# Kernel tuning notes

Measured on AMD Instinct MI355X. Metric: run time of the kernel, lower is better.

The kernel has to match this reference:

```python
import jax, jax.numpy as jnp
import numpy as np

TTT_LR = 0.01
LN_EPS = 1e-5


def setup_inputs() -> dict:
    key = jax.random.key(0)
    ks = jax.random.split(key, 4)
    B, S, D, DS = 4, 2048, 1024, 64
    sc = 1.0 / np.sqrt(D).astype(np.float32)
    return {
        "x": jax.random.normal(ks[0], (B, S, D), dtype=jnp.float32),
        "Wk": jax.random.normal(ks[1], (DS, D), dtype=jnp.float32) * sc,
        "bk": jnp.zeros((DS,), jnp.float32),
        "Wv": jax.random.normal(ks[2], (D, D), dtype=jnp.float32) * sc,
        "bv": jnp.zeros((D,), jnp.float32),
        "Wq": jax.random.normal(ks[3], (DS, D), dtype=jnp.float32) * sc,
        "bq": jnp.zeros((DS,), jnp.float32),
        "gamma": jnp.ones((D,), jnp.float32),
        "beta": jnp.zeros((D,), jnp.float32),
    }


def reference(x, Wk, bk, Wv, bv, Wq, bq, gamma, beta):
    B, S, D = x.shape
    DS = Wk.shape[0]
    # LayerNorm over last dim
    mu = jnp.mean(x, axis=-1, keepdims=True)
    var = jnp.mean((x - mu) ** 2, axis=-1, keepdims=True)
    h = (x - mu) * jax.lax.rsqrt(var + LN_EPS) * gamma + beta
    # projections: keys/queries (B,S,DS), values (B,S,D)
    keys = jnp.einsum('bsd,ed->bse', h, Wk) + bk
    values = jnp.einsum('bsd,ed->bse', h, Wv) + bv
    queries = jnp.einsum('bsd,ed->bse', h, Wq) + bq

    def step(W, qkv):
        # W: (B, D, DS) fast-weight state
        q_t, k_t, v_t = qkv  # (B,DS), (B,DS), (B,D)
        y_t = jnp.einsum('bds,bs->bd', W, q_t)      # read with query
        pred = jnp.einsum('bds,bs->bd', W, k_t)     # predict with key
        err = pred - v_t                             # (B, D)
        W = W - TTT_LR * err[:, :, None] * k_t[:, None, :]  # rank-1 grad step
        return W, y_t

    W0 = jnp.zeros((B, D, DS), x.dtype)
    # scan over time: inputs as (S, B, ...)
    qs = jnp.swapaxes(queries, 0, 1)
    ks_ = jnp.swapaxes(keys, 0, 1)
    vs = jnp.swapaxes(values, 0, 1)
    _, ys = jax.lax.scan(step, W0, (qs, ks_, vs))   # ys: (S, B, D)
    y = jnp.swapaxes(ys, 0, 1)
    return x + y
```

## Files before the change

### kernel.cpp

```cpp
#include <hip/hip_runtime.h>
#include <hip/hip_bf16.h>

#define TTT_LR 0.01f
#define LN_EPS 1e-5f

#define BB 4
#define SS 2048
#define DD 1024
#define DSZ 64
#define CHUNK 64
#define NC (SS / CHUNK)
#define NCAT 1152
#define NCVT (NCAT * DD / 4 / 256)
#define MiB (1024ull * 1024ull)

typedef __hip_bfloat16 bf16;
typedef __bf16 bf16x8 __attribute__((ext_vector_type(8)));
typedef float f32x4 __attribute__((ext_vector_type(4)));

__device__ __forceinline__ void gload_lds16(const void* g, void* l) {
    __builtin_amdgcn_global_load_lds(
        (const __attribute__((address_space(1))) unsigned int*)g,
        (__attribute__((address_space(3))) unsigned int*)l, 16, 0, 0);
}

__global__ __launch_bounds__(256) void pre_kernel(
    const float* __restrict__ Wk, const float* __restrict__ Wq,
    const float* __restrict__ Wv, bf16* __restrict__ Wcat,
    const float* __restrict__ x, const float* __restrict__ gamma,
    const float* __restrict__ beta, bf16* __restrict__ hb)
{
    __shared__ float wsum[4], wsum2[4];
    const int tid = threadIdx.x;

    if (blockIdx.x < NCVT) {
        const int i = blockIdx.x * 256 + tid;
        const int idx = i * 4;
        const int row = idx >> 10, col = idx & 1023;
        const float* src = (row < 64)  ? (Wk + (size_t)row * DD)
                         : (row < 128) ? (Wq + (size_t)(row - 64) * DD)
                                       : (Wv + (size_t)(row - 128) * DD);
        float4 v = *reinterpret_cast<const float4*>(src + col);
        bf16 h4[4] = {__float2bfloat16(v.x), __float2bfloat16(v.y),
                      __float2bfloat16(v.z), __float2bfloat16(v.w)};
        *reinterpret_cast<ushort4*>(Wcat + idx) = *reinterpret_cast<ushort4*>(h4);
        return;
    }

    const int row = blockIdx.x - NCVT;
    const int lane = tid & 63, wave = tid >> 6;

    float4 v0 = *reinterpret_cast<const float4*>(x + (size_t)row * DD + tid * 4);
    float s = v0.x + v0.y + v0.z + v0.w;
    float s2 = fmaf(v0.x, v0.x, fmaf(v0.y, v0.y, fmaf(v0.z, v0.z, v0.w * v0.w)));
    #pragma unroll
    for (int off = 32; off > 0; off >>= 1) {
        s  += __shfl_down(s, off, 64);
        s2 += __shfl_down(s2, off, 64);
    }
    if (lane == 0) { wsum[wave] = s; wsum2[wave] = s2; }
    __syncthreads();
    s  = wsum[0] + wsum[1] + wsum[2] + wsum[3];
    s2 = wsum2[0] + wsum2[1] + wsum2[2] + wsum2[3];
    const float mu = s * (1.0f / DD);
    const float rs = rsqrtf(s2 * (1.0f / DD) - mu * mu + LN_EPS);

    float4 g  = *reinterpret_cast<const float4*>(gamma + tid * 4);
    float4 be = *reinterpret_cast<const float4*>(beta + tid * 4);
    bf16 h4[4];
    h4[0] = __float2bfloat16((v0.x - mu) * rs * g.x + be.x);
    h4[1] = __float2bfloat16((v0.y - mu) * rs * g.y + be.y);
    h4[2] = __float2bfloat16((v0.z - mu) * rs * g.z + be.z);
    h4[3] = __float2bfloat16((v0.w - mu) * rs * g.w + be.w);
    *reinterpret_cast<ushort4*>(hb + (size_t)row * DD + tid * 4) =
        *reinterpret_cast<ushort4*>(h4);
}

__global__ __launch_bounds__(256) void kqv_kernel(
    const bf16* __restrict__ h, const bf16* __restrict__ Wcat,
    const float* __restrict__ bk, const float* __restrict__ bq,
    const float* __restrict__ bv,
    float* __restrict__ kbuf, float* __restrict__ qbuf, bf16* __restrict__ vbuf16)
{
    __shared__ bf16 Ash[64 * 64];
    __shared__ bf16 Bsh[128 * 64];
    const int tid = threadIdx.x, lane = tid & 63, wave = tid >> 6;
    const int m = lane & 15, quad = lane >> 4;
    const int wr = wave >> 1, wc = wave & 1;

    const int id = blockIdx.x;
    const int tile = (id & 7) * 144 + (id >> 3);
    const int mtile = tile / 9;
    const int ntile = tile % 9;
    const int m0 = mtile * 64;
    const int n0 = ntile * 128;

    const int srow = wave * 8 + (lane >> 3);
    const int scb = lane & 7;

    f32x4 acc[2][4] = {};

    for (int k0 = 0; k0 < DD; k0 += 64) {
        __syncthreads();
        #pragma unroll
        for (int i = 0; i < 2; ++i) {
            const int row = i * 32 + srow;
            const int g16 = scb ^ (row & 7);
            gload_lds16(h    + (size_t)(m0 + row) * DD + k0 + g16 * 8,
                        (char*)Ash + (size_t)(i * 32 + wave * 8) * 128);
        }
        #pragma unroll
        for (int i = 0; i < 4; ++i) {
            const int row = i * 32 + srow;
            const int g16 = scb ^ (row & 7);
            gload_lds16(Wcat + (size_t)(n0 + row) * DD + k0 + g16 * 8,
                        (char*)Bsh + (size_t)(i * 32 + wave * 8) * 128);
        }
        __syncthreads();
        #pragma unroll
        for (int ks = 0; ks < 2; ++ks) {
            bf16x8 af[2], bfr[4];
            #pragma unroll
            for (int mt = 0; mt < 2; ++mt) {
                const int row = wr * 32 + mt * 16 + m;
                const int kb = (ks * 4 + quad) ^ (row & 7);
                af[mt] = *reinterpret_cast<const bf16x8*>(&Ash[row * 64 + kb * 8]);
            }
            #pragma unroll
            for (int nt = 0; nt < 4; ++nt) {
                const int row = wc * 64 + nt * 16 + m;
                const int kb = (ks * 4 + quad) ^ (row & 7);
                bfr[nt] = *reinterpret_cast<const bf16x8*>(&Bsh[row * 64 + kb * 8]);
            }
            #pragma unroll
            for (int mt = 0; mt < 2; ++mt)
                #pragma unroll
                for (int nt = 0; nt < 4; ++nt)
                    acc[mt][nt] = __builtin_amdgcn_mfma_f32_16x16x32_bf16(
                        af[mt], bfr[nt], acc[mt][nt], 0, 0, 0);
        }
    }

    #pragma unroll
    for (int nt = 0; nt < 4; ++nt) {
        const int n = n0 + wc * 64 + nt * 16 + m;
        if (n < 64) {
            const float bias = bk[n];
            #pragma unroll
            for (int mt = 0; mt < 2; ++mt) {
                const int row = m0 + wr * 32 + mt * 16 + quad * 4;
                #pragma unroll
                for (int r = 0; r < 4; ++r)
                    kbuf[(size_t)(row + r) * DSZ + n] = acc[mt][nt][r] + bias;
            }
        } else if (n < 128) {
            const float bias = bq[n - 64];
            #pragma unroll
            for (int mt = 0; mt < 2; ++mt) {
                const int row = m0 + wr * 32 + mt * 16 + quad * 4;
                #pragma unroll
                for (int r = 0; r < 4; ++r)
                    qbuf[(size_t)(row + r) * DSZ + (n - 64)] = acc[mt][nt][r] + bias;
            }
        } else {
            const float bias = bv[n - 128];
            #pragma unroll
            for (int mt = 0; mt < 2; ++mt) {
                const int row = m0 + wr * 32 + mt * 16 + quad * 4;
                #pragma unroll
                for (int r = 0; r < 4; ++r)
                    vbuf16[(size_t)(row + r) * DD + (n - 128)] =
                        __float2bfloat16(acc[mt][nt][r] + bias);
            }
        }
    }
}

__global__ __launch_bounds__(256) void prep_kernel(
    const float* __restrict__ kbuf, const float* __restrict__ qbuf,
    bf16* __restrict__ Tb16, bf16* __restrict__ Wb16,
    bf16* __restrict__ AMb16, bf16* __restrict__ Qtb16)
{
    __shared__ bf16 K16[64 * 72];
    __shared__ bf16 Kt16[64 * 72];
    __shared__ bf16 Q16[64 * 72];
    __shared__ bf16 Astl[64 * 72];
    __shared__ bf16 Minv16[64 * 72];
    __shared__ bf16 MinvT16[64 * 72];
    __shared__ bf16 BnegT[64 * 72];
    __shared__ float Gf[64 * 65];
    __shared__ float Mf[64 * 65];

    const int c = blockIdx.x, b = blockIdx.y;
    const int tid = threadIdx.x, lane = tid & 63, w = tid >> 6;
    const int m = lane & 15, quad = lane >> 4;
    const float* kp = kbuf + ((size_t)b * SS + c * 64) * DSZ;
    const float* qp = qbuf + ((size_t)b * SS + c * 64) * DSZ;
    const size_t cb = ((size_t)b * NC + c) * 4096;

    #pragma unroll
    for (int it = 0; it < 4; ++it) {
        const int f4 = tid + it * 256;
        const int t = f4 >> 4;
        const int s = (f4 & 15) * 4;
        float4 kv = *reinterpret_cast<const float4*>(kp + t * DSZ + s);
        float4 qv = *reinterpret_cast<const float4*>(qp + t * DSZ + s);
        bf16 kb4[4] = {__float2bfloat16(kv.x), __float2bfloat16(kv.y),
                       __float2bfloat16(kv.z), __float2bfloat16(kv.w)};
        bf16 qb4[4] = {__float2bfloat16(qv.x), __float2bfloat16(qv.y),
                       __float2bfloat16(qv.z), __float2bfloat16(qv.w)};
        *reinterpret_cast<ushort4*>(&K16[t * 72 + s]) = *reinterpret_cast<ushort4*>(kb4);
        *reinterpret_cast<ushort4*>(&Q16[t * 72 + s]) = *reinterpret_cast<ushort4*>(qb4);
        #pragma unroll
        for (int i = 0; i < 4; ++i) Kt16[(s + i) * 72 + t] = kb4[i];
    }
    __syncthreads();

    bf16x8 afK[2], afQ[2], bfK[4][2];
    #pragma unroll
    for (int ks = 0; ks < 2; ++ks) {
        afK[ks] = *reinterpret_cast<const bf16x8*>(&K16[(w * 16 + m) * 72 + ks * 32 + quad * 8]);
        afQ[ks] = *reinterpret_cast<const bf16x8*>(&Q16[(w * 16 + m) * 72 + ks * 32 + quad * 8]);
        #pragma unroll
        for (int nt = 0; nt < 4; ++nt)
            bfK[nt][ks] = *reinterpret_cast<const bf16x8*>(&K16[(nt * 16 + m) * 72 + ks * 32 + quad * 8]);
    }
    f32x4 gacc[4] = {}, aacc[4] = {};
    #pragma unroll
    for (int ks = 0; ks < 2; ++ks)
        #pragma unroll
        for (int nt = 0; nt < 4; ++nt) {
            gacc[nt] = __builtin_amdgcn_mfma_f32_16x16x32_bf16(afK[ks], bfK[nt][ks], gacc[nt], 0, 0, 0);
            aacc[nt] = __builtin_amdgcn_mfma_f32_16x16x32_bf16(afQ[ks], bfK[nt][ks], aacc[nt], 0, 0, 0);
        }
    #pragma unroll
    for (int nt = 0; nt < 4; ++nt)
        #pragma unroll
        for (int r = 0; r < 4; ++r) {
            const int t = w * 16 + quad * 4 + r, j = nt * 16 + m;
            Gf[t * 65 + j] = TTT_LR * gacc[nt][r];
            Astl[t * 72 + j] = __float2bfloat16(j < t ? aacc[nt][r] : 0.f);
        }
    __syncthreads();

    if (tid < 64) {
        for (int t = 0; t < 64; ++t) {
            float acc = (t == tid) ? 1.f : 0.f;
            for (int i = 0; i < t; ++i)
                acc = fmaf(-Gf[t * 65 + i], Mf[i * 65 + tid], acc);
            Mf[t * 65 + tid] = acc;
        }
    }
    __syncthreads();

    #pragma unroll
    for (int it = 0; it < 16; ++it) {
        const int e = tid + it * 256;
        const int t = e >> 6, j = e & 63;
        const bf16 vb = __float2bfloat16(TTT_LR * Mf[t * 65 + j]);
        Minv16[t * 72 + j] = vb;
        MinvT16[j * 72 + t] = vb;
    }
    __syncthreads();

    bf16x8 afM[2], afA[2], afKt[2], bfKt[4][2], bfMt[4][2];
    #pragma unroll
    for (int ks = 0; ks < 2; ++ks) {
        afM[ks]  = *reinterpret_cast<const bf16x8*>(&Minv16[(w * 16 + m) * 72 + ks * 32 + quad * 8]);
        afA[ks]  = *reinterpret_cast<const bf16x8*>(&Astl[(w * 16 + m) * 72 + ks * 32 + quad * 8]);
        afKt[ks] = *reinterpret_cast<const bf16x8*>(&Kt16[(w * 16 + m) * 72 + ks * 32 + quad * 8]);
        #pragma unroll
        for (int nt = 0; nt < 4; ++nt) {
            bfKt[nt][ks] = *reinterpret_cast<const bf16x8*>(&Kt16[(nt * 16 + m) * 72 + ks * 32 + quad * 8]);
            bfMt[nt][ks] = *reinterpret_cast<const bf16x8*>(&MinvT16[(nt * 16 + m) * 72 + ks * 32 + quad * 8]);
        }
    }
    f32x4 bacc[4] = {};
    #pragma unroll
    for (int ks = 0; ks < 2; ++ks)
        #pragma unroll
        for (int nt = 0; nt < 4; ++nt)
            bacc[nt] = __builtin_amdgcn_mfma_f32_16x16x32_bf16(afM[ks], bfKt[nt][ks], bacc[nt], 0, 0, 0);
    #pragma unroll
    for (int nt = 0; nt < 4; ++nt)
        #pragma unroll
        for (int r = 0; r < 4; ++r) {
            const int t = w * 16 + quad * 4 + r, s = nt * 16 + m;
            BnegT[s * 72 + t] = __float2bfloat16(-bacc[nt][r]);
        }
    __syncthreads();

    f32x4 qtacc[4], amacc[4] = {}, tacc[4] = {}, wacc[4] = {};
    #pragma unroll
    for (int nt = 0; nt < 4; ++nt)
        #pragma unroll
        for (int r = 0; r < 4; ++r)
            qtacc[nt][r] = qp[(w * 16 + quad * 4 + r) * DSZ + nt * 16 + m];
    #pragma unroll
    for (int ks = 0; ks < 2; ++ks)
        #pragma unroll
        for (int nt = 0; nt < 4; ++nt) {
            const bf16x8 bfBn = *reinterpret_cast<const bf16x8*>(
                &BnegT[(nt * 16 + m) * 72 + ks * 32 + quad * 8]);
            qtacc[nt] = __builtin_amdgcn_mfma_f32_16x16x32_bf16(afA[ks], bfBn, qtacc[nt], 0, 0, 0);
            amacc[nt] = __builtin_amdgcn_mfma_f32_16x16x32_bf16(afA[ks], bfMt[nt][ks], amacc[nt], 0, 0, 0);
            tacc[nt]  = __builtin_amdgcn_mfma_f32_16x16x32_bf16(afKt[ks], bfBn, tacc[nt], 0, 0, 0);
            wacc[nt]  = __builtin_amdgcn_mfma_f32_16x16x32_bf16(afKt[ks], bfMt[nt][ks], wacc[nt], 0, 0, 0);
        }
    #pragma unroll
    for (int nt = 0; nt < 4; ++nt)
        #pragma unroll
        for (int r = 0; r < 4; ++r) {
            const int row = w * 16 + quad * 4 + r, col = nt * 16 + m;
            Qtb16[cb + row * 64 + col] = __float2bfloat16(qtacc[nt][r]);
            AMb16[cb + row * 64 + col] = __float2bfloat16(amacc[nt][r]);
            Tb16[cb + row * 64 + col]  = __float2bfloat16(tacc[nt][r]);
            Wb16[cb + row * 64 + col]  = __float2bfloat16(wacc[nt][r]);
        }
}

struct ChunkRegs {
    bf16x8 T0, T1, W0, W1, A0, A1, Q0, Q1;
    alignas(8) unsigned short va[4], vb[4];
    float xld[4];
};

__global__ __launch_bounds__(256) void scan2_kernel(
    const bf16* __restrict__ Tb16, const bf16* __restrict__ Wb16,
    const bf16* __restrict__ AMb16, const bf16* __restrict__ Qtb16,
    const bf16* __restrict__ v16, const float* __restrict__ x,
    float* __restrict__ out)
{
    __shared__ bf16 Zsh[2][16][72];
    __shared__ bf16 Vsh[2][16][72];
    const int id = blockIdx.x;
    const int tile = (id & 7) * 32 + (id >> 3);
    const int b = tile >> 6, dblk = tile & 63;
    const int tid = threadIdx.x, lane = tid & 63, w = tid >> 6;
    const int m = lane & 15, quad = lane >> 4;
    const int d0 = dblk * 16;
    const int arow = w * 16 + m;
    const int trow = w * 16 + quad * 4;

    const bool vact = tid < 128;
    const int vj2 = (tid & 31) * 2;
    const int vd = (tid >> 5) * 4;

    f32x4 zacc = {0.f, 0.f, 0.f, 0.f};
    for (int i = tid; i < 16 * 72; i += 256)
        (&Zsh[0][0][0])[i] = __float2bfloat16(0.f);

    auto load_chunk = [&](int c, ChunkRegs& R) {
        const size_t cb = ((size_t)b * NC + c) * 4096;
        const size_t rowbase = (size_t)b * SS + (size_t)c * 64;
        R.T0 = *reinterpret_cast<const bf16x8*>(Tb16 + cb + arow * 64 + quad * 8);
        R.T1 = *reinterpret_cast<const bf16x8*>(Tb16 + cb + arow * 64 + 32 + quad * 8);
        R.W0 = *reinterpret_cast<const bf16x8*>(Wb16 + cb + arow * 64 + quad * 8);
        R.W1 = *reinterpret_cast<const bf16x8*>(Wb16 + cb + arow * 64 + 32 + quad * 8);
        R.A0 = *reinterpret_cast<const bf16x8*>(AMb16 + cb + arow * 64 + quad * 8);
        R.A1 = *reinterpret_cast<const bf16x8*>(AMb16 + cb + arow * 64 + 32 + quad * 8);
        R.Q0 = *reinterpret_cast<const bf16x8*>(Qtb16 + cb + arow * 64 + quad * 8);
        R.Q1 = *reinterpret_cast<const bf16x8*>(Qtb16 + cb + arow * 64 + 32 + quad * 8);
        if (vact) {
            *reinterpret_cast<uint2*>(R.va) = *reinterpret_cast<const uint2*>(
                v16 + (rowbase + vj2) * DD + d0 + vd);
            *reinterpret_cast<uint2*>(R.vb) = *reinterpret_cast<const uint2*>(
                v16 + (rowbase + vj2 + 1) * DD + d0 + vd);
        }
        const size_t gbase = (rowbase + trow) * DD + d0 + m;
        #pragma unroll
        for (int r = 0; r < 4; ++r) R.xld[r] = x[gbase + (size_t)r * DD];
    };

    auto stage_v = [&](const ChunkRegs& R, int buf) {
        if (vact) {
            #pragma unroll
            for (int i = 0; i < 4; ++i) {
                const unsigned int pack =
                    (unsigned int)R.va[i] | ((unsigned int)R.vb[i] << 16);
                *reinterpret_cast<unsigned int*>(&Vsh[buf][vd + i][vj2]) = pack;
            }
        }
    };

    auto compute = [&](const ChunkRegs& R, int c, int buf) {
        const size_t gbase = ((size_t)b * SS + (size_t)c * 64 + trow) * DD + d0 + m;
        const bf16x8 z0 = *reinterpret_cast<const bf16x8*>(&Zsh[buf][m][quad * 8]);
        const bf16x8 z1 = *reinterpret_cast<const bf16x8*>(&Zsh[buf][m][32 + quad * 8]);
        const bf16x8 v0 = *reinterpret_cast<const bf16x8*>(&Vsh[buf][m][quad * 8]);
        const bf16x8 v1 = *reinterpret_cast<const bf16x8*>(&Vsh[buf][m][32 + quad * 8]);

        zacc = __builtin_amdgcn_mfma_f32_16x16x32_bf16(R.T0, z0, zacc, 0, 0, 0);
        zacc = __builtin_amdgcn_mfma_f32_16x16x32_bf16(R.T1, z1, zacc, 0, 0, 0);
        zacc = __builtin_amdgcn_mfma_f32_16x16x32_bf16(R.W0, v0, zacc, 0, 0, 0);
        zacc = __builtin_amdgcn_mfma_f32_16x16x32_bf16(R.W1, v1, zacc, 0, 0, 0);

        f32x4 y = {0.f, 0.f, 0.f, 0.f};
        y = __builtin_amdgcn_mfma_f32_16x16x32_bf16(R.Q0, z0, y, 0, 0, 0);
        y = __builtin_amdgcn_mfma_f32_16x16x32_bf16(R.Q1, z1, y, 0, 0, 0);
        y = __builtin_amdgcn_mfma_f32_16x16x32_bf16(R.A0, v0, y, 0, 0, 0);
        y = __builtin_amdgcn_mfma_f32_16x16x32_bf16(R.A1, v1, y, 0, 0, 0);

        alignas(8) bf16 zb[4];
        #pragma unroll
        for (int r = 0; r < 4; ++r) zb[r] = __float2bfloat16(zacc[r]);
        *reinterpret_cast<uint2*>(&Zsh[buf ^ 1][m][trow]) =
            *reinterpret_cast<uint2*>(zb);

        #pragma unroll
        for (int r = 0; r < 4; ++r)
            out[gbase + (size_t)r * DD] = R.xld[r] + y[r];
    };

    ChunkRegs R0, R1;
    load_chunk(0, R0);
    for (int c = 0; c < NC; c += 2) {
        stage_v(R0, 0);
        __syncthreads();
        load_chunk(c + 1, R1);
        compute(R0, c, 0);
        stage_v(R1, 1);
        __syncthreads();
        if (c + 2 < NC) load_chunk(c + 2, R0);
        compute(R1, c + 1, 1);
    }
}

extern "C" void kernel_launch(void* const* d_in, const int* in_sizes, int n_in,
                              void* d_out, int out_size, void* d_ws, size_t ws_size,
                              hipStream_t stream)
{
    const float* x     = (const float*)d_in[0];
    const float* Wk    = (const float*)d_in[1];
    const float* bk    = (const float*)d_in[2];
    const float* Wv    = (const float*)d_in[3];
    const float* bv    = (const float*)d_in[4];
    const float* Wq    = (const float*)d_in[5];
    const float* bq    = (const float*)d_in[6];
    const float* gamma = (const float*)d_in[7];
    const float* beta  = (const float*)d_in[8];

    char* ws = (char*)d_ws;
    const size_t WCAT_B = (size_t)NCAT * DD * 2;
    bf16*  hb    = (bf16*)ws;
    bf16*  Tb16  = (bf16*)(ws + 0 * MiB);
    bf16*  Qtb16 = (bf16*)(ws + 1 * MiB);
    bf16*  Wb16  = (bf16*)(ws + 2 * MiB);
    bf16*  AMb16 = (bf16*)(ws + 3 * MiB);
    bf16*  Wcat  = (bf16*)(ws + 16 * MiB);
    float* kbuf  = (float*)(ws + 16 * MiB + WCAT_B);
    float* qbuf  = (float*)(ws + 18 * MiB + WCAT_B);
    bf16*  v16   = (bf16*)(ws + 20 * MiB + WCAT_B);

    pre_kernel<<<NCVT + BB * SS, 256, 0, stream>>>(
        Wk, Wq, Wv, Wcat, x, gamma, beta, hb);
    kqv_kernel<<<dim3(1152), 256, 0, stream>>>(
        hb, Wcat, bk, bq, bv, kbuf, qbuf, v16);
    prep_kernel<<<dim3(NC, BB), 256, 0, stream>>>(
        kbuf, qbuf, Tb16, Wb16, AMb16, Qtb16);
    scan2_kernel<<<dim3(256), 256, 0, stream>>>(
        Tb16, Wb16, AMb16, Qtb16, v16, x, (float*)d_out);
}
```

Measured before the change: 208.2 us.

## Deepen scan prefetch of V/x and use LDS-only barrier in scan kernel

Splits the per-chunk register bundle into matrix operands and value/residual operands, and prefetches the value and x loads two chunks ahead instead of one. Replaces __syncthreads with a barrier that waits only on LDS counters, so outstanding global loads need not drain at each barrier. It also moves the Z store to LDS ahead of the output MFMAs to shorten the serial chain. The deeper prefetch raises register pressure, and correctness now depends on the LDS-only wait covering all shared-memory hazards.

```diff
diff --git a/kernel.cpp b/kernel.cpp
--- a/kernel.cpp
+++ b/kernel.cpp
@@ -22,6 +22,12 @@
     __builtin_amdgcn_global_load_lds(
         (const __attribute__((address_space(1))) unsigned int*)g,
         (__attribute__((address_space(3))) unsigned int*)l, 16, 0, 0);
+}
+
+__device__ __forceinline__ void barrier_lgkm() {
+    asm volatile("s_waitcnt lgkmcnt(0)" ::: "memory");
+    __builtin_amdgcn_s_barrier();
+    asm volatile("" ::: "memory");
 }
 
 __global__ __launch_bounds__(256) void pre_kernel(
@@ -319,8 +325,8 @@
         }
 }
 
-struct ChunkRegs {
-    bf16x8 T0, T1, W0, W1, A0, A1, Q0, Q1;
+struct MRegs { bf16x8 T0, T1, W0, W1, A0, A1, Q0, Q1; };
+struct VRegs {
     alignas(8) unsigned short va[4], vb[4];
     float xld[4];
 };
@@ -350,9 +356,8 @@
     for (int i = tid; i < 16 * 72; i += 256)
         (&Zsh[0][0][0])[i] = __float2bfloat16(0.f);
 
-    auto load_chunk = [&](int c, ChunkRegs& R) {
+    auto load_m = [&](int c, MRegs& R) {
         const size_t cb = ((size_t)b * NC + c) * 4096;
-        const size_t rowbase = (size_t)b * SS + (size_t)c * 64;
         R.T0 = *reinterpret_cast<const bf16x8*>(Tb16 + cb + arow * 64 + quad * 8);
         R.T1 = *reinterpret_cast<const bf16x8*>(Tb16 + cb + arow * 64 + 32 + quad * 8);
         R.W0 = *reinterpret_cast<const bf16x8*>(Wb16 + cb + arow * 64 + quad * 8);
@@ -361,30 +366,33 @@
         R.A1 = *reinterpret_cast<const bf16x8*>(AMb16 + cb + arow * 64 + 32 + quad * 8);
         R.Q0 = *reinterpret_cast<const bf16x8*>(Qtb16 + cb + arow * 64 + quad * 8);
         R.Q1 = *reinterpret_cast<const bf16x8*>(Qtb16 + cb + arow * 64 + 32 + quad * 8);
+    };
+
+    auto load_v = [&](int c, VRegs& V) {
+        const size_t rowbase = (size_t)b * SS + (size_t)c * 64;
         if (vact) {
-            *reinterpret_cast<uint2*>(R.va) = *reinterpret_cast<const uint2*>(
+            *reinterpret_cast<uint2*>(V.va) = *reinterpret_cast<const uint2*>(
                 v16 + (rowbase + vj2) * DD + d0 + vd);
-            *reinterpret_cast<uint2*>(R.vb) = *reinterpret_cast<const uint2*>(
+            *reinterpret_cast<uint2*>(V.vb) = *reinterpret_cast<const uint2*>(
                 v16 + (rowbase + vj2 + 1) * DD + d0 + vd);
         }
         const size_t gbase = (rowbase + trow) * DD + d0 + m;
         #pragma unroll
-        for (int r = 0; r < 4; ++r) R.xld[r] = x[gbase + (size_t)r * DD];
+        for (int r = 0; r < 4; ++r) V.xld[r] = x[gbase + (size_t)r * DD];
     };
 
-    auto stage_v = [&](const ChunkRegs& R, int buf) {
+    auto stage_v = [&](const VRegs& V, int buf) {
         if (vact) {
             #pragma unroll
             for (int i = 0; i < 4; ++i) {
                 const unsigned int pack =
-                    (unsigned int)R.va[i] | ((unsigned int)R.vb[i] << 16);
+                    (unsigned int)V.va[i] | ((unsigned int)V.vb[i] << 16);
                 *reinterpret_cast<unsigned int*>(&Vsh[buf][vd + i][vj2]) = pack;
             }
         }
     };
 
-    auto compute = [&](const ChunkRegs& R, int c, int buf) {
-        const size_t gbase = ((size_t)b * SS + (size_t)c * 64 + trow) * DD + d0 + m;
+    auto compute = [&](const MRegs& R, const VRegs& V, int c, int buf) {
         const bf16x8 z0 = *reinterpret_cast<const bf16x8*>(&Zsh[buf][m][quad * 8]);
         const bf16x8 z1 = *reinterpret_cast<const bf16x8*>(&Zsh[buf][m][32 + quad * 8]);
         const bf16x8 v0 = *reinterpret_cast<const bf16x8*>(&Vsh[buf][m][quad * 8]);
@@ -394,6 +402,12 @@
         zacc = __builtin_amdgcn_mfma_f32_16x16x32_bf16(R.T1, z1, zacc, 0, 0, 0);
         zacc = __builtin_amdgcn_mfma_f32_16x16x32_bf16(R.W0, v0, zacc, 0, 0, 0);
         zacc = __builtin_amdgcn_mfma_f32_16x16x32_bf16(R.W1, v1, zacc, 0, 0, 0);
+
+        alignas(8) bf16 zb[4];
+        #pragma unroll
+        for (int r = 0; r < 4; ++r) zb[r] = __float2bfloat16(zacc[r]);
+        *reinterpret_cast<uint2*>(&Zsh[buf ^ 1][m][trow]) =
+            *reinterpret_cast<uint2*>(zb);
 
         f32x4 y = {0.f, 0.f, 0.f, 0.f};
         y = __builtin_amdgcn_mfma_f32_16x16x32_bf16(R.Q0, z0, y, 0, 0, 0);
@@ -401,28 +415,29 @@
         y = __builtin_amdgcn_mfma_f32_16x16x32_bf16(R.A0, v0, y, 0, 0, 0);
         y = __builtin_amdgcn_mfma_f32_16x16x32_bf16(R.A1, v1, y, 0, 0, 0);
 
-        alignas(8) bf16 zb[4];
-        #pragma unroll
-        for (int r = 0; r < 4; ++r) zb[r] = __float2bfloat16(zacc[r]);
-        *reinterpret_cast<uint2*>(&Zsh[buf ^ 1][m][trow]) =
-            *reinterpret_cast<uint2*>(zb);
-
+        const size_t gbase = ((size_t)b * SS + (size_t)c * 64 + trow) * DD + d0 + m;
         #pragma unroll
         for (int r = 0; r < 4; ++r)
-            out[gbase + (size_t)r * DD] = R.xld[r] + y[r];
+            out[gbase + (size_t)r * DD] = V.xld[r] + y[r];
     };
 
-    ChunkRegs R0, R1;
-    load_chunk(0, R0);
+    VRegs V0, V1;
+    MRegs M0, M1;
+    load_v(0, V0);
+    load_v(1, V1);
+    load_m(0, M0);
     for (int c = 0; c < NC; c += 2) {
-        stage_v(R0, 0);
-        __syncthreads();
-        load_chunk(c + 1, R1);
-        compute(R0, c, 0);
-        stage_v(R1, 1);
-        __syncthreads();
-        if (c + 2 < NC) load_chunk(c + 2, R0);
-        compute(R1, c + 1, 1);
+        stage_v(V0, 0);
+        barrier_lgkm();
+        load_m(c + 1, M1);
+        compute(M0, V0, c, 0);
+        if (c + 2 < NC) load_v(c + 2, V0);
+
+        stage_v(V1, 1);
+        barrier_lgkm();
+        if (c + 2 < NC) load_m(c + 2, M0);
+        compute(M1, V1, c + 1, 1);
+        if (c + 3 < NC) load_v(c + 3, V1);
     }
 }
 
```

New measurement: 205.1 us. No clear change (-1.5%).
